# Kernel tuning notes

Hardware: AMD Instinct MI355X
Metric: run time of the kernel (lower is better)

## Reference

```python
import jax, jax.numpy as jnp
import numpy as np

ALPHA = 0.005
SCALE = 0.001
DELTA = 0.1
MAX_ITER = 50
EARLY = True


def setup_inputs() -> dict:
    key = jax.random.key(0)
    k1, k2, k3 = jax.random.split(key, 3)
    B, S, M, N = 32, 8, 512, 512
    x = jax.random.uniform(k1, (B, S, N), dtype=jnp.float32)
    A = jax.random.normal(k2, (B, S, M, N), dtype=jnp.float32) * 0.1
    b = jax.random.uniform(k3, (B, S, M), dtype=jnp.float32)
    return {"x": x, "A": A, "b": b}


def reference(x, A, b):
    # x: [B,S,N] primal iterate; A: [B,S,M,N] constraint matrices; b: [B,S,M]
    B, S = b.shape[0], b.shape[1]
    active0 = jnp.ones((B, S), dtype=bool)

    def body(carry, _):
        x_, active, stopped = carry
        # torch loop runs an iteration only while any(active) and not early-stopped
        run = jnp.any(active) & (~stopped)
        # Ax - b, clamped at 0 -> per-constraint violation
        Ax = jnp.einsum('bsn,bsmn->bsm', x_, A)          # [B,S,M]
        viol = jnp.clip(Ax - b, 0.0)
        new_active = jnp.sum(viol, axis=-1) >= DELTA      # ~(total < delta)
        stop_early = jnp.asarray(EARLY) & (~jnp.any(new_active))
        g = jnp.einsum('bsm,bsmn->bsn', viol, A)          # penalty gradient [B,S,N]
        lr = ALPHA / (1.0 + SCALE * g)
        x_upd = jnp.where(new_active[..., None], x_ - lr * g, x_)
        x_upd = jnp.clip(x_upd, 0.0)                      # clamp applied even to inactive rows
        # early stop happens BEFORE the update/clamp in the torch code
        x_new = jnp.where(stop_early, x_, x_upd)
        x_out = jnp.where(run, x_new, x_)
        active_out = jnp.where(run, new_active, active)
        stopped_out = stopped | (run & stop_early)
        return (x_out, active_out, stopped_out), None

    # torch: break when count > max_iter after increment -> up to max_iter+1 updates
    init = (x, active0, jnp.array(False))
    (x_final, _, _), _ = jax.lax.scan(body, init, None, length=MAX_ITER + 1)
    return x_final
```

## Files before the change

kernel.cpp:

```cpp
#include <hip/hip_runtime.h>

#define ALPHA 0.005f
#define SCALE 0.001f
#define DELTA 0.1f
#define MAXIT 51

constexpr int N = 512;
constexpr int M = 512;
constexpr int NTHREADS = 1024;
constexpr int NWAVES = NTHREADS / 64;
constexpr int MPW = M / NWAVES;
constexpr int NROWS = 256;
constexpr size_t WS_NEEDED = (size_t)NROWS * M * N * 2;

constexpr int CACHE_M0 = 416;
constexpr int CACHE_KK0 = 26;

template<int CTRL>
__device__ __forceinline__ float dpp_mov(float v) {
    return __int_as_float(__builtin_amdgcn_update_dpp(
        0, __float_as_int(v), CTRL, 0xF, 0xF, true));
}

__device__ __forceinline__ float wave_sum_u(float d) {
    d += dpp_mov<0x111>(d);
    d += dpp_mov<0x112>(d);
    d += dpp_mov<0x114>(d);
    d += dpp_mov<0x118>(d);
    d += dpp_mov<0x142>(d);
    d += dpp_mov<0x143>(d);
    return __int_as_float(__builtin_amdgcn_readlane(__float_as_int(d), 63));
}

__device__ __forceinline__ float dot8(const float4& a, const float4& c,
                                      const float4& xa, const float4& xb) {
    return a.x*xa.x + a.y*xa.y + a.z*xa.z + a.w*xa.w
         + c.x*xb.x + c.y*xb.y + c.z*xb.z + c.w*xb.w;
}

__device__ __forceinline__ unsigned pack2_bf16(float f0, float f1) {
    unsigned a = __float_as_uint(f0); a += 0x7fffu + ((a >> 16) & 1u);
    unsigned b = __float_as_uint(f1); b += 0x7fffu + ((b >> 16) & 1u);
    return (a >> 16) | (b & 0xffff0000u);
}
__device__ __forceinline__ float bflo(unsigned u) { return __uint_as_float(u << 16); }
__device__ __forceinline__ float bfhi(unsigned u) { return __uint_as_float(u & 0xffff0000u); }

__device__ __forceinline__ void unpack4(uint2 u, float4& f) {
    f.x = bflo(u.x); f.y = bfhi(u.x); f.z = bflo(u.y); f.w = bfhi(u.y);
}

__global__ __launch_bounds__(NTHREADS, 4)
void lva_bf16_kernel(const float* __restrict__ x_in,
                     const float* __restrict__ A,
                     const float* __restrict__ bvec,
                     float* __restrict__ x_out,
                     unsigned short* __restrict__ wsA)
{
    __shared__ __align__(16) float b_lds[M];
    __shared__ __align__(16) float g_lds[NWAVES * N];
    __shared__ float sv_lds[NWAVES];
    __shared__ int bc_active;
    __shared__ __align__(16) uint2 A_lds[96 * 128];

    const int tid  = threadIdx.x;
    const int lane = tid & 63;
    const int w    = tid >> 6;
    const int r    = blockIdx.x;

    if (tid < M) b_lds[tid] = bvec[(size_t)r * M + tid];

    const int n0 = lane * 4;
    const int n1 = 256 + lane * 4;

    const float* xrow = x_in + (size_t)r * N;
    float4 xa = *(const float4*)(xrow + n0);
    float4 xb = *(const float4*)(xrow + n1);

    const float* Ablk = A + (size_t)r * M * N + (size_t)w * N;
    unsigned short* Wblk = wsA + (size_t)r * M * N + (size_t)w * N;

    __syncthreads();

    bool alive = true;

    {
        float4 ga = make_float4(0.f, 0.f, 0.f, 0.f);
        float4 gb = make_float4(0.f, 0.f, 0.f, 0.f);
        float sviol = 0.f;

        #define STROW(j, aj, cj) do {                                               \
            if (kk + (j) >= CACHE_KK0) {                                            \
                const int rl = w + 16 * (kk + (j)) - CACHE_M0;                      \
                A_lds[rl * 128 + lane]      = make_uint2(pack2_bf16(aj.x, aj.y),    \
                                                         pack2_bf16(aj.z, aj.w));   \
                A_lds[rl * 128 + 64 + lane] = make_uint2(pack2_bf16(cj.x, cj.y),    \
                                                         pack2_bf16(cj.z, cj.w));   \
            } else {                                                                \
                unsigned short* q = Wblk + (size_t)(kk + (j)) * (16 * N);           \
                *(uint2*)(q + n0) = make_uint2(pack2_bf16(aj.x, aj.y),              \
                                               pack2_bf16(aj.z, aj.w));             \
                *(uint2*)(q + n1) = make_uint2(pack2_bf16(cj.x, cj.y),              \
                                               pack2_bf16(cj.z, cj.w));             \
            }                                                                       \
        } while (0)

        #pragma unroll 1
        for (int kk = 0; kk < MPW; kk += 4) {
            const float* p0 = Ablk + (size_t)(kk + 0) * (16 * N);
            const float* p1 = Ablk + (size_t)(kk + 1) * (16 * N);
            const float* p2 = Ablk + (size_t)(kk + 2) * (16 * N);
            const float* p3 = Ablk + (size_t)(kk + 3) * (16 * N);
            float4 a0 = *(const float4*)(p0 + n0), c0 = *(const float4*)(p0 + n1);
            float4 a1 = *(const float4*)(p1 + n0), c1 = *(const float4*)(p1 + n1);
            float4 a2 = *(const float4*)(p2 + n0), c2 = *(const float4*)(p2 + n1);
            float4 a3 = *(const float4*)(p3 + n0), c3 = *(const float4*)(p3 + n1);
            STROW(0, a0, c0); STROW(1, a1, c1); STROW(2, a2, c2); STROW(3, a3, c3);
            float bb0 = b_lds[w + 16 * (kk + 0)];
            float bb1 = b_lds[w + 16 * (kk + 1)];
            float bb2 = b_lds[w + 16 * (kk + 2)];
            float bb3 = b_lds[w + 16 * (kk + 3)];
            float d0 = wave_sum_u(dot8(a0, c0, xa, xb));
            float d1 = wave_sum_u(dot8(a1, c1, xa, xb));
            float d2 = wave_sum_u(dot8(a2, c2, xa, xb));
            float d3 = wave_sum_u(dot8(a3, c3, xa, xb));
            float v0 = fmaxf(d0 - bb0, 0.f);
            float v1 = fmaxf(d1 - bb1, 0.f);
            float v2 = fmaxf(d2 - bb2, 0.f);
            float v3 = fmaxf(d3 - bb3, 0.f);
            sviol += v0 + v1 + v2 + v3;
            ga.x += v0*a0.x + v1*a1.x + v2*a2.x + v3*a3.x;
            ga.y += v0*a0.y + v1*a1.y + v2*a2.y + v3*a3.y;
            ga.z += v0*a0.z + v1*a1.z + v2*a2.z + v3*a3.z;
            ga.w += v0*a0.w + v1*a1.w + v2*a2.w + v3*a3.w;
            gb.x += v0*c0.x + v1*c1.x + v2*c2.x + v3*c3.x;
            gb.y += v0*c0.y + v1*c1.y + v2*c2.y + v3*c3.y;
            gb.z += v0*c0.z + v1*c1.z + v2*c2.z + v3*c3.z;
            gb.w += v0*c0.w + v1*c1.w + v2*c2.w + v3*c3.w;
        }
        #undef STROW

        if (lane == 0) sv_lds[w] = sviol;
        *(float4*)(&g_lds[w * N + n0]) = ga;
        *(float4*)(&g_lds[w * N + n1]) = gb;
        __syncthreads();
        if (tid == 0) {
            float s = 0.f;
            #pragma unroll
            for (int i = 0; i < NWAVES; ++i) s += sv_lds[i];
            bc_active = (s >= DELTA) ? 1 : 0;
        }
        if (tid < N) {
            float s = 0.f;
            #pragma unroll
            for (int i = 0; i < NWAVES; ++i) s += g_lds[i * N + tid];
            g_lds[tid] = s;
        }
        __syncthreads();
        if (!bc_active) {
            alive = false;
        } else {
            float4 gfa = *(const float4*)(&g_lds[n0]);
            float4 gfb = *(const float4*)(&g_lds[n1]);
            xa.x = fmaxf(xa.x - (ALPHA / (1.f + SCALE*gfa.x)) * gfa.x, 0.f);
            xa.y = fmaxf(xa.y - (ALPHA / (1.f + SCALE*gfa.y)) * gfa.y, 0.f);
            xa.z = fmaxf(xa.z - (ALPHA / (1.f + SCALE*gfa.z)) * gfa.z, 0.f);
            xa.w = fmaxf(xa.w - (ALPHA / (1.f + SCALE*gfa.w)) * gfa.w, 0.f);
            xb.x = fmaxf(xb.x - (ALPHA / (1.f + SCALE*gfb.x)) * gfb.x, 0.f);
            xb.y = fmaxf(xb.y - (ALPHA / (1.f + SCALE*gfb.y)) * gfb.y, 0.f);
            xb.z = fmaxf(xb.z - (ALPHA / (1.f + SCALE*gfb.z)) * gfb.z, 0.f);
            xb.w = fmaxf(xb.w - (ALPHA / (1.f + SCALE*gfb.w)) * gfb.w, 0.f);
        }
    }

    const int h = lane >> 5;
    const int s = lane & 31;
    __syncthreads();
    if (w == 0) {
        *(float4*)(&g_lds[n0]) = xa;
        *(float4*)(&g_lds[n1]) = xb;
    }
    __syncthreads();
    float4 xf0 = *(const float4*)(&g_lds[  0 + s * 4]);
    float4 xf1 = *(const float4*)(&g_lds[128 + s * 4]);
    float4 xf2 = *(const float4*)(&g_lds[256 + s * 4]);
    float4 xf3 = *(const float4*)(&g_lds[384 + s * 4]);
    __syncthreads();

    if (alive) {
        const uint2* Wp = (const uint2*)(wsA + (size_t)r * M * N)
                          + (w + 16 * h) * 128 + s;
        const int mb = w + 16 * h;
        const int xadr = (lane ^ 32) << 2;

        uint2 c0, c1, c2, c3, p0, p1, p2, p3;

        #define LOADG(b0, b1, b2, b3, Gn) do {  \
            b0 = Wp[(Gn) * 4096];               \
            b1 = Wp[(Gn) * 4096 + 32];          \
            b2 = Wp[(Gn) * 4096 + 64];          \
            b3 = Wp[(Gn) * 4096 + 96];          \
        } while (0)

        #define COMPUTE(b0, b1, b2, b3, G) do {                               \
            float4 f0, f1, f2, f3;                                            \
            unpack4(b0, f0); unpack4(b1, f1);                                 \
            unpack4(b2, f2); unpack4(b3, f3);                                 \
            float d = f0.x*xf0.x + f0.y*xf0.y + f0.z*xf0.z + f0.w*xf0.w       \
                    + f1.x*xf1.x + f1.y*xf1.y + f1.z*xf1.z + f1.w*xf1.w       \
                    + f2.x*xf2.x + f2.y*xf2.y + f2.z*xf2.z + f2.w*xf2.w       \
                    + f3.x*xf3.x + f3.y*xf3.y + f3.z*xf3.z + f3.w*xf3.w;      \
            d += dpp_mov<0xB1>(d);            \
            d += dpp_mov<0x4E>(d);            \
            d += dpp_mov<0x141>(d);           \
            d += dpp_mov<0x140>(d);           \
            d += __int_as_float(__builtin_amdgcn_ds_swizzle(                  \
                     __float_as_int(d), 0x401F));        \
            float v = fmaxf(d - b_lds[mb + 32 * (G)], 0.f);                   \
            sviol += v;                                                       \
            g0.x += v*f0.x; g0.y += v*f0.y; g0.z += v*f0.z; g0.w += v*f0.w;   \
            g1.x += v*f1.x; g1.y += v*f1.y; g1.z += v*f1.z; g1.w += v*f1.w;   \
            g2.x += v*f2.x; g2.y += v*f2.y; g2.z += v*f2.z; g2.w += v*f2.w;   \
            g3.x += v*f3.x; g3.y += v*f3.y; g3.z += v*f3.z; g3.w += v*f3.w;   \
        } while (0)

        #define MRG(x) (x) += __int_as_float(                                 \
            __builtin_amdgcn_ds_bpermute(xadr, __float_as_int(x)))

        LOADG(c0, c1, c2, c3, 0);

        #pragma unroll 1
        for (int t = 1; t < MAXIT; ++t) {
            float4 g0 = make_float4(0.f, 0.f, 0.f, 0.f);
            float4 g1 = make_float4(0.f, 0.f, 0.f, 0.f);
            float4 g2 = make_float4(0.f, 0.f, 0.f, 0.f);
            float4 g3 = make_float4(0.f, 0.f, 0.f, 0.f);
            float sviol = 0.f;

            #pragma unroll 1
            for (int G = 0; G < 12; G += 2) {
                LOADG(p0, p1, p2, p3, G + 1);
                COMPUTE(c0, c1, c2, c3, G);
                LOADG(c0, c1, c2, c3, G + 2);
                COMPUTE(p0, p1, p2, p3, G + 1);
            }
            COMPUTE(c0, c1, c2, c3, 12);
            LOADG(c0, c1, c2, c3, 0);

            {
                const int base = mb * 128 + s;
                p0 = A_lds[base]; p1 = A_lds[base + 32];
                p2 = A_lds[base + 64]; p3 = A_lds[base + 96];
                COMPUTE(p0, p1, p2, p3, 13);
            }
            {
                const int base = (mb + 32) * 128 + s;
                p0 = A_lds[base]; p1 = A_lds[base + 32];
                p2 = A_lds[base + 64]; p3 = A_lds[base + 96];
                COMPUTE(p0, p1, p2, p3, 14);
            }
            {
                const int base = (mb + 64) * 128 + s;
                p0 = A_lds[base]; p1 = A_lds[base + 32];
                p2 = A_lds[base + 64]; p3 = A_lds[base + 96];
                COMPUTE(p0, p1, p2, p3, 15);
            }

            MRG(g0.x); MRG(g0.y); MRG(g0.z); MRG(g0.w);
            MRG(g1.x); MRG(g1.y); MRG(g1.z); MRG(g1.w);
            MRG(g2.x); MRG(g2.y); MRG(g2.z); MRG(g2.w);
            MRG(g3.x); MRG(g3.y); MRG(g3.z); MRG(g3.w);
            MRG(sviol);

            if (h == 0) {
                const int gb = w * N + s * 4;
                *(float4*)(&g_lds[gb      ]) = g0;
                *(float4*)(&g_lds[gb + 128]) = g1;
                *(float4*)(&g_lds[gb + 256]) = g2;
                *(float4*)(&g_lds[gb + 384]) = g3;
                if (s == 0) sv_lds[w] = sviol;
            }
            __syncthreads();
            if (tid == 0) {
                float sacc = 0.f;
                #pragma unroll
                for (int i = 0; i < NWAVES; ++i) sacc += sv_lds[i];
                bc_active = (sacc >= DELTA) ? 1 : 0;
            }
            if (tid < N) {
                float sacc = 0.f;
                #pragma unroll
                for (int i = 0; i < NWAVES; ++i) sacc += g_lds[i * N + tid];
                g_lds[tid] = sacc;
            }
            __syncthreads();
            if (!bc_active) break;

            float4 q0 = *(const float4*)(&g_lds[  0 + s * 4]);
            float4 q1 = *(const float4*)(&g_lds[128 + s * 4]);
            float4 q2 = *(const float4*)(&g_lds[256 + s * 4]);
            float4 q3 = *(const float4*)(&g_lds[384 + s * 4]);
            xf0.x = fmaxf(xf0.x - (ALPHA / (1.f + SCALE*q0.x)) * q0.x, 0.f);
            xf0.y = fmaxf(xf0.y - (ALPHA / (1.f + SCALE*q0.y)) * q0.y, 0.f);
            xf0.z = fmaxf(xf0.z - (ALPHA / (1.f + SCALE*q0.z)) * q0.z, 0.f);
            xf0.w = fmaxf(xf0.w - (ALPHA / (1.f + SCALE*q0.w)) * q0.w, 0.f);
            xf1.x = fmaxf(xf1.x - (ALPHA / (1.f + SCALE*q1.x)) * q1.x, 0.f);
            xf1.y = fmaxf(xf1.y - (ALPHA / (1.f + SCALE*q1.y)) * q1.y, 0.f);
            xf1.z = fmaxf(xf1.z - (ALPHA / (1.f + SCALE*q1.z)) * q1.z, 0.f);
            xf1.w = fmaxf(xf1.w - (ALPHA / (1.f + SCALE*q1.w)) * q1.w, 0.f);
            xf2.x = fmaxf(xf2.x - (ALPHA / (1.f + SCALE*q2.x)) * q2.x, 0.f);
            xf2.y = fmaxf(xf2.y - (ALPHA / (1.f + SCALE*q2.y)) * q2.y, 0.f);
            xf2.z = fmaxf(xf2.z - (ALPHA / (1.f + SCALE*q2.z)) * q2.z, 0.f);
            xf2.w = fmaxf(xf2.w - (ALPHA / (1.f + SCALE*q2.w)) * q2.w, 0.f);
            xf3.x = fmaxf(xf3.x - (ALPHA / (1.f + SCALE*q3.x)) * q3.x, 0.f);
            xf3.y = fmaxf(xf3.y - (ALPHA / (1.f + SCALE*q3.y)) * q3.y, 0.f);
            xf3.z = fmaxf(xf3.z - (ALPHA / (1.f + SCALE*q3.z)) * q3.z, 0.f);
            xf3.w = fmaxf(xf3.w - (ALPHA / (1.f + SCALE*q3.w)) * q3.w, 0.f);
            __syncthreads();
        }
        #undef LOADG
        #undef COMPUTE
        #undef MRG
    }

    if (w == 0 && h == 0) {
        float* orow = x_out + (size_t)r * N + s * 4;
        *(float4*)(orow +   0) = xf0;
        *(float4*)(orow + 128) = xf1;
        *(float4*)(orow + 256) = xf2;
        *(float4*)(orow + 384) = xf3;
    }
}

__global__ __launch_bounds__(NTHREADS, 4)
void lva_kernel(const float* __restrict__ x_in,
                const float* __restrict__ A,
                const float* __restrict__ bvec,
                float* __restrict__ x_out)
{
    __shared__ float b_lds[M];
    __shared__ float g_lds[NWAVES * N];
    __shared__ float sv_lds[NWAVES];
    __shared__ int bc_active;

    const int tid  = threadIdx.x;
    const int lane = tid & 63;
    const int w    = tid >> 6;
    const int r    = blockIdx.x;

    if (tid < M) b_lds[tid] = bvec[(size_t)r * M + tid];

    const int n0 = lane * 4;
    const int n1 = 256 + lane * 4;

    const float* xrow = x_in + (size_t)r * N;
    float4 xa = *(const float4*)(xrow + n0);
    float4 xb = *(const float4*)(xrow + n1);

    const float* Ablk = A + (size_t)r * M * N + (size_t)w * N;

    __syncthreads();

    for (int t = 0; t < MAXIT; ++t) {
        float4 ga = make_float4(0.f, 0.f, 0.f, 0.f);
        float4 gb = make_float4(0.f, 0.f, 0.f, 0.f);
        float sviol = 0.f;

        #pragma unroll 1
        for (int kk = 0; kk < MPW; kk += 4) {
            const float* p0 = Ablk + (size_t)(kk + 0) * (16 * N);
            const float* p1 = Ablk + (size_t)(kk + 1) * (16 * N);
            const float* p2 = Ablk + (size_t)(kk + 2) * (16 * N);
            const float* p3 = Ablk + (size_t)(kk + 3) * (16 * N);
            float4 a0 = *(const float4*)(p0 + n0), c0 = *(const float4*)(p0 + n1);
            float4 a1 = *(const float4*)(p1 + n0), c1 = *(const float4*)(p1 + n1);
            float4 a2 = *(const float4*)(p2 + n0), c2 = *(const float4*)(p2 + n1);
            float4 a3 = *(const float4*)(p3 + n0), c3 = *(const float4*)(p3 + n1);
            float bb0 = b_lds[w + 16 * (kk + 0)];
            float bb1 = b_lds[w + 16 * (kk + 1)];
            float bb2 = b_lds[w + 16 * (kk + 2)];
            float bb3 = b_lds[w + 16 * (kk + 3)];
            float d0 = wave_sum_u(dot8(a0, c0, xa, xb));
            float d1 = wave_sum_u(dot8(a1, c1, xa, xb));
            float d2 = wave_sum_u(dot8(a2, c2, xa, xb));
            float d3 = wave_sum_u(dot8(a3, c3, xa, xb));
            float v0 = fmaxf(d0 - bb0, 0.f);
            float v1 = fmaxf(d1 - bb1, 0.f);
            float v2 = fmaxf(d2 - bb2, 0.f);
            float v3 = fmaxf(d3 - bb3, 0.f);
            sviol += v0 + v1 + v2 + v3;
            ga.x += v0*a0.x + v1*a1.x + v2*a2.x + v3*a3.x;
            ga.y += v0*a0.y + v1*a1.y + v2*a2.y + v3*a3.y;
            ga.z += v0*a0.z + v1*a1.z + v2*a2.z + v3*a3.z;
            ga.w += v0*a0.w + v1*a1.w + v2*a2.w + v3*a3.w;
            gb.x += v0*c0.x + v1*c1.x + v2*c2.x + v3*c3.x;
            gb.y += v0*c0.y + v1*c1.y + v2*c2.y + v3*c3.y;
            gb.z += v0*c0.z + v1*c1.z + v2*c2.z + v3*c3.z;
            gb.w += v0*c0.w + v1*c1.w + v2*c2.w + v3*c3.w;
        }

        if (lane == 0) sv_lds[w] = sviol;
        *(float4*)(&g_lds[w * N + n0]) = ga;
        *(float4*)(&g_lds[w * N + n1]) = gb;
        __syncthreads();
        if (tid == 0) {
            float sacc = 0.f;
            #pragma unroll
            for (int i = 0; i < NWAVES; ++i) sacc += sv_lds[i];
            bc_active = (sacc >= DELTA) ? 1 : 0;
        }
        if (tid < N) {
            float sacc = 0.f;
            #pragma unroll
            for (int i = 0; i < NWAVES; ++i) sacc += g_lds[i * N + tid];
            g_lds[tid] = sacc;
        }
        __syncthreads();
        if (!bc_active) break;

        float4 gfa = *(const float4*)(&g_lds[n0]);
        float4 gfb = *(const float4*)(&g_lds[n1]);
        xa.x = fmaxf(xa.x - (ALPHA / (1.f + SCALE*gfa.x)) * gfa.x, 0.f);
        xa.y = fmaxf(xa.y - (ALPHA / (1.f + SCALE*gfa.y)) * gfa.y, 0.f);
        xa.z = fmaxf(xa.z - (ALPHA / (1.f + SCALE*gfa.z)) * gfa.z, 0.f);
        xa.w = fmaxf(xa.w - (ALPHA / (1.f + SCALE*gfa.w)) * gfa.w, 0.f);
        xb.x = fmaxf(xb.x - (ALPHA / (1.f + SCALE*gfb.x)) * gfb.x, 0.f);
        xb.y = fmaxf(xb.y - (ALPHA / (1.f + SCALE*gfb.y)) * gfb.y, 0.f);
        xb.z = fmaxf(xb.z - (ALPHA / (1.f + SCALE*gfb.z)) * gfb.z, 0.f);
        xb.w = fmaxf(xb.w - (ALPHA / (1.f + SCALE*gfb.w)) * gfb.w, 0.f);
        __syncthreads();
    }

    float* orow = x_out + (size_t)r * N;
    if (w == 0) {
        *(float4*)(orow + n0) = xa;
        *(float4*)(orow + n1) = xb;
    }
}

extern "C" void kernel_launch(void* const* d_in, const int* in_sizes, int n_in,
                              void* d_out, int out_size, void* d_ws, size_t ws_size,
                              hipStream_t stream)
{
    const float* x  = (const float*)d_in[0];
    const float* A  = (const float*)d_in[1];
    const float* b  = (const float*)d_in[2];
    float* out      = (float*)d_out;

    if (ws_size >= WS_NEEDED) {
        lva_bf16_kernel<<<dim3(NROWS), dim3(NTHREADS), 0, stream>>>(
            x, A, b, out, (unsigned short*)d_ws);
    } else {
        lva_kernel<<<dim3(NROWS), dim3(NTHREADS), 0, stream>>>(x, A, b, out);
    }
}
```

Before: 1.146 ms.

## Cache bf16 A rows in registers and LDS, cut workspace reads per iteration

```diff
diff --git a/kernel.cpp b/kernel.cpp
--- a/kernel.cpp
+++ b/kernel.cpp
@@ -13,8 +13,7 @@
 constexpr int NROWS = 256;
 constexpr size_t WS_NEEDED = (size_t)NROWS * M * N * 2;
 
-constexpr int CACHE_M0 = 416;
-constexpr int CACHE_KK0 = 26;
+constexpr int CACHE_M0 = 384;
 
 template<int CTRL>
 __device__ __forceinline__ float dpp_mov(float v) {
@@ -59,6 +58,7 @@
 {
     __shared__ __align__(16) float b_lds[M];
     __shared__ __align__(16) float g_lds[NWAVES * N];
+    __shared__ __align__(16) float gred[N];
     __shared__ float sv_lds[NWAVES];
     __shared__ int bc_active;
     __shared__ __align__(16) uint2 A_lds[96 * 128];
@@ -67,6 +67,9 @@
     const int lane = tid & 63;
     const int w    = tid >> 6;
     const int r    = blockIdx.x;
+    const int h    = lane >> 5;
+    const int s    = lane & 31;
+    const int xadr = (lane ^ 32) << 2;
 
     if (tid < M) b_lds[tid] = bvec[(size_t)r * M + tid];
 
@@ -83,85 +86,147 @@
     __syncthreads();
 
     bool alive = true;
+
+    uint2 q0a = make_uint2(0,0), q0b = q0a, q0c = q0a, q0d = q0a;
+    uint2 q1a = q0a, q1b = q0a, q1c = q0a, q1d = q0a;
+    uint2 q2a = q0a, q2b = q0a, q2c = q0a, q2d = q0a;
+    uint2 q3a = q0a, q3b = q0a, q3c = q0a, q3d = q0a;
+    uint2 q4a = q0a, q4b = q0a, q4c = q0a, q4d = q0a;
 
     {
         float4 ga = make_float4(0.f, 0.f, 0.f, 0.f);
         float4 gb = make_float4(0.f, 0.f, 0.f, 0.f);
         float sviol = 0.f;
-
-        #define STROW(j, aj, cj) do {                                               \
-            if (kk + (j) >= CACHE_KK0) {                                            \
-                const int rl = w + 16 * (kk + (j)) - CACHE_M0;                      \
-                A_lds[rl * 128 + lane]      = make_uint2(pack2_bf16(aj.x, aj.y),    \
-                                                         pack2_bf16(aj.z, aj.w));   \
-                A_lds[rl * 128 + 64 + lane] = make_uint2(pack2_bf16(cj.x, cj.y),    \
-                                                         pack2_bf16(cj.z, cj.w));   \
-            } else {                                                                \
-                unsigned short* q = Wblk + (size_t)(kk + (j)) * (16 * N);           \
-                *(uint2*)(q + n0) = make_uint2(pack2_bf16(aj.x, aj.y),              \
-                                               pack2_bf16(aj.z, aj.w));             \
-                *(uint2*)(q + n1) = make_uint2(pack2_bf16(cj.x, cj.y),              \
-                                               pack2_bf16(cj.z, cj.w));             \
-            }                                                                       \
+        float4 a0, a1, a2, a3, c0, c1, c2, c3;
+
+        #define LOADA4(KK) do {                                               \
+            const float* P0 = Ablk + (size_t)((KK) + 0) * (16 * N);           \
+            const float* P1 = Ablk + (size_t)((KK) + 1) * (16 * N);           \
+            const float* P2 = Ablk + (size_t)((KK) + 2) * (16 * N);           \
+            const float* P3 = Ablk + (size_t)((KK) + 3) * (16 * N);           \
+            a0 = *(const float4*)(P0 + n0); c0 = *(const float4*)(P0 + n1);   \
+            a1 = *(const float4*)(P1 + n0); c1 = *(const float4*)(P1 + n1);   \
+            a2 = *(const float4*)(P2 + n0); c2 = *(const float4*)(P2 + n1);   \
+            a3 = *(const float4*)(P3 + n0); c3 = *(const float4*)(P3 + n1);   \
+        } while (0)
+
+        #define DOTGRAD4(KK) do {                                             \
+            float bb0 = b_lds[w + 16 * ((KK) + 0)];                           \
+            float bb1 = b_lds[w + 16 * ((KK) + 1)];                           \
+            float bb2 = b_lds[w + 16 * ((KK) + 2)];                           \
+            float bb3 = b_lds[w + 16 * ((KK) + 3)];                           \
+            float d0 = wave_sum_u(dot8(a0, c0, xa, xb));                      \
+            float d1 = wave_sum_u(dot8(a1, c1, xa, xb));                      \
+            float d2 = wave_sum_u(dot8(a2, c2, xa, xb));                      \
+            float d3 = wave_sum_u(dot8(a3, c3, xa, xb));                      \
+            float v0 = fmaxf(d0 - bb0, 0.f);                                  \
+            float v1 = fmaxf(d1 - bb1, 0.f);                                  \
+            float v2 = fmaxf(d2 - bb2, 0.f);                                  \
+            float v3 = fmaxf(d3 - bb3, 0.f);                                  \
+            sviol += v0 + v1 + v2 + v3;                                       \
+            ga.x += v0*a0.x + v1*a1.x + v2*a2.x + v3*a3.x;                    \
+            ga.y += v0*a0.y + v1*a1.y + v2*a2.y + v3*a3.y;                    \
+            ga.z += v0*a0.z + v1*a1.z + v2*a2.z + v3*a3.z;                    \
+            ga.w += v0*a0.w + v1*a1.w + v2*a2.w + v3*a3.w;                    \
+            gb.x += v0*c0.x + v1*c1.x + v2*c2.x + v3*c3.x;                    \
+            gb.y += v0*c0.y + v1*c1.y + v2*c2.y + v3*c3.y;                    \
+            gb.z += v0*c0.z + v1*c1.z + v2*c2.z + v3*c3.z;                    \
+            gb.w += v0*c0.w + v1*c1.w + v2*c2.w + v3*c3.w;                    \
+        } while (0)
+
+        #define WS1(J, AJ, CJ) do {                                           \
+            unsigned short* q = Wblk + (size_t)(J) * (16 * N);                \
+            *(uint2*)(q + n0) = make_uint2(pack2_bf16(AJ.x, AJ.y),            \
+                                           pack2_bf16(AJ.z, AJ.w));           \
+            *(uint2*)(q + n1) = make_uint2(pack2_bf16(CJ.x, CJ.y),            \
+                                           pack2_bf16(CJ.z, CJ.w));           \
+        } while (0)
+
+        #define LDS1(J, AJ, CJ) do {                                          \
+            const int rl = w + 16 * (J) - CACHE_M0;                           \
+            A_lds[rl * 128 + lane]      = make_uint2(pack2_bf16(AJ.x, AJ.y),  \
+                                                     pack2_bf16(AJ.z, AJ.w)); \
+            A_lds[rl * 128 + 64 + lane] = make_uint2(pack2_bf16(CJ.x, CJ.y),  \
+                                                     pack2_bf16(CJ.z, CJ.w)); \
+        } while (0)
+
+        #define BPERM(v) (unsigned)__builtin_amdgcn_ds_bpermute(xadr, (int)(v))
+
+        #define CAPE(Q, AJ, CJ) do {                                          \
+            unsigned lo0 = pack2_bf16(AJ.x, AJ.y), lo1 = pack2_bf16(AJ.z, AJ.w); \
+            unsigned hi0 = pack2_bf16(CJ.x, CJ.y), hi1 = pack2_bf16(CJ.z, CJ.w); \
+            unsigned rl0 = BPERM(lo0), rl1 = BPERM(lo1);                      \
+            unsigned rh0 = BPERM(hi0), rh1 = BPERM(hi1);                      \
+            if (h == 0) {                                                     \
+                Q##a = make_uint2(lo0, lo1); Q##b = make_uint2(rl0, rl1);     \
+                Q##c = make_uint2(hi0, hi1); Q##d = make_uint2(rh0, rh1);     \
+            }                                                                 \
+        } while (0)
+        #define CAPO(Q, AJ, CJ) do {                                          \
+            unsigned lo0 = pack2_bf16(AJ.x, AJ.y), lo1 = pack2_bf16(AJ.z, AJ.w); \
+            unsigned hi0 = pack2_bf16(CJ.x, CJ.y), hi1 = pack2_bf16(CJ.z, CJ.w); \
+            unsigned rl0 = BPERM(lo0), rl1 = BPERM(lo1);                      \
+            unsigned rh0 = BPERM(hi0), rh1 = BPERM(hi1);                      \
+            if (h == 1) {                                                     \
+                Q##a = make_uint2(rl0, rl1); Q##b = make_uint2(lo0, lo1);     \
+                Q##c = make_uint2(rh0, rh1); Q##d = make_uint2(hi0, hi1);     \
+            }                                                                 \
         } while (0)
 
         #pragma unroll 1
-        for (int kk = 0; kk < MPW; kk += 4) {
-            const float* p0 = Ablk + (size_t)(kk + 0) * (16 * N);
-            const float* p1 = Ablk + (size_t)(kk + 1) * (16 * N);
-            const float* p2 = Ablk + (size_t)(kk + 2) * (16 * N);
-            const float* p3 = Ablk + (size_t)(kk + 3) * (16 * N);
-            float4 a0 = *(const float4*)(p0 + n0), c0 = *(const float4*)(p0 + n1);
-            float4 a1 = *(const float4*)(p1 + n0), c1 = *(const float4*)(p1 + n1);
-            float4 a2 = *(const float4*)(p2 + n0), c2 = *(const float4*)(p2 + n1);
-            float4 a3 = *(const float4*)(p3 + n0), c3 = *(const float4*)(p3 + n1);
-            STROW(0, a0, c0); STROW(1, a1, c1); STROW(2, a2, c2); STROW(3, a3, c3);
-            float bb0 = b_lds[w + 16 * (kk + 0)];
-            float bb1 = b_lds[w + 16 * (kk + 1)];
-            float bb2 = b_lds[w + 16 * (kk + 2)];
-            float bb3 = b_lds[w + 16 * (kk + 3)];
-            float d0 = wave_sum_u(dot8(a0, c0, xa, xb));
-            float d1 = wave_sum_u(dot8(a1, c1, xa, xb));
-            float d2 = wave_sum_u(dot8(a2, c2, xa, xb));
-            float d3 = wave_sum_u(dot8(a3, c3, xa, xb));
-            float v0 = fmaxf(d0 - bb0, 0.f);
-            float v1 = fmaxf(d1 - bb1, 0.f);
-            float v2 = fmaxf(d2 - bb2, 0.f);
-            float v3 = fmaxf(d3 - bb3, 0.f);
-            sviol += v0 + v1 + v2 + v3;
-            ga.x += v0*a0.x + v1*a1.x + v2*a2.x + v3*a3.x;
-            ga.y += v0*a0.y + v1*a1.y + v2*a2.y + v3*a3.y;
-            ga.z += v0*a0.z + v1*a1.z + v2*a2.z + v3*a3.z;
-            ga.w += v0*a0.w + v1*a1.w + v2*a2.w + v3*a3.w;
-            gb.x += v0*c0.x + v1*c1.x + v2*c2.x + v3*c3.x;
-            gb.y += v0*c0.y + v1*c1.y + v2*c2.y + v3*c3.y;
-            gb.z += v0*c0.z + v1*c1.z + v2*c2.z + v3*c3.z;
-            gb.w += v0*c0.w + v1*c1.w + v2*c2.w + v3*c3.w;
-        }
-        #undef STROW
+        for (int kk = 0; kk < 16; kk += 4) {
+            LOADA4(kk);
+            WS1(kk + 0, a0, c0); WS1(kk + 1, a1, c1);
+            WS1(kk + 2, a2, c2); WS1(kk + 3, a3, c3);
+            DOTGRAD4(kk);
+        }
+        LOADA4(16);
+        CAPE(q0, a0, c0); CAPO(q0, a1, c1);
+        CAPE(q1, a2, c2); CAPO(q1, a3, c3);
+        DOTGRAD4(16);
+        LOADA4(20);
+        CAPE(q2, a0, c0); CAPO(q2, a1, c1);
+        CAPE(q3, a2, c2); CAPO(q3, a3, c3);
+        DOTGRAD4(20);
+        LOADA4(24);
+        LDS1(24, a0, c0); LDS1(25, a1, c1);
+        LDS1(26, a2, c2); LDS1(27, a3, c3);
+        DOTGRAD4(24);
+        LOADA4(28);
+        LDS1(28, a0, c0); LDS1(29, a1, c1);
+        CAPE(q4, a2, c2); CAPO(q4, a3, c3);
+        DOTGRAD4(28);
+
+        #undef LOADA4
+        #undef WS1
+        #undef LDS1
+        #undef CAPE
+        #undef CAPO
+        #undef BPERM
+        #undef DOTGRAD4
 
         if (lane == 0) sv_lds[w] = sviol;
         *(float4*)(&g_lds[w * N + n0]) = ga;
         *(float4*)(&g_lds[w * N + n1]) = gb;
         __syncthreads();
         if (tid == 0) {
-            float s = 0.f;
+            float sacc = 0.f;
             #pragma unroll
-            for (int i = 0; i < NWAVES; ++i) s += sv_lds[i];
-            bc_active = (s >= DELTA) ? 1 : 0;
+            for (int i = 0; i < NWAVES; ++i) sacc += sv_lds[i];
+            bc_active = (sacc >= DELTA) ? 1 : 0;
         }
         if (tid < N) {
-            float s = 0.f;
+            float sacc = 0.f;
             #pragma unroll
-            for (int i = 0; i < NWAVES; ++i) s += g_lds[i * N + tid];
-            g_lds[tid] = s;
+            for (int i = 0; i < NWAVES; ++i) sacc += g_lds[i * N + tid];
+            gred[tid] = sacc;
         }
         __syncthreads();
         if (!bc_active) {
             alive = false;
         } else {
-            float4 gfa = *(const float4*)(&g_lds[n0]);
-            float4 gfb = *(const float4*)(&g_lds[n1]);
+            float4 gfa = *(const float4*)(&gred[n0]);
+            float4 gfb = *(const float4*)(&gred[n1]);
             xa.x = fmaxf(xa.x - (ALPHA / (1.f + SCALE*gfa.x)) * gfa.x, 0.f);
             xa.y = fmaxf(xa.y - (ALPHA / (1.f + SCALE*gfa.y)) * gfa.y, 0.f);
             xa.z = fmaxf(xa.z - (ALPHA / (1.f + SCALE*gfa.z)) * gfa.z, 0.f);
@@ -173,8 +238,6 @@
         }
     }
 
-    const int h = lane >> 5;
-    const int s = lane & 31;
     __syncthreads();
     if (w == 0) {
         *(float4*)(&g_lds[n0]) = xa;
@@ -191,7 +254,6 @@
         const uint2* Wp = (const uint2*)(wsA + (size_t)r * M * N)
                           + (w + 16 * h) * 128 + s;
         const int mb = w + 16 * h;
-        const int xadr = (lane ^ 32) << 2;
 
         uint2 c0, c1, c2, c3, p0, p1, p2, p3;
 
@@ -237,34 +299,40 @@
             float4 g3 = make_float4(0.f, 0.f, 0.f, 0.f);
             float sviol = 0.f;
 
-            #pragma unroll 1
-            for (int G = 0; G < 12; G += 2) {
-                LOADG(p0, p1, p2, p3, G + 1);
-                COMPUTE(c0, c1, c2, c3, G);
-                LOADG(c0, c1, c2, c3, G + 2);
-                COMPUTE(p0, p1, p2, p3, G + 1);
-            }
-            COMPUTE(c0, c1, c2, c3, 12);
-            LOADG(c0, c1, c2, c3, 0);
+            LOADG(p0, p1, p2, p3, 1); COMPUTE(c0, c1, c2, c3, 0);
+            LOADG(c0, c1, c2, c3, 2); COMPUTE(p0, p1, p2, p3, 1);
+            LOADG(p0, p1, p2, p3, 3); COMPUTE(c0, c1, c2, c3, 2);
+            LOADG(c0, c1, c2, c3, 4); COMPUTE(p0, p1, p2, p3, 3);
+            LOADG(p0, p1, p2, p3, 5); COMPUTE(c0, c1, c2, c3, 4);
+            LOADG(c0, c1, c2, c3, 6); COMPUTE(p0, p1, p2, p3, 5);
+            LOADG(p0, p1, p2, p3, 7); COMPUTE(c0, c1, c2, c3, 6);
+            LOADG(c0, c1, c2, c3, 0); COMPUTE(p0, p1, p2, p3, 7);
+
+            COMPUTE(q0a, q0b, q0c, q0d,  8);
+            COMPUTE(q1a, q1b, q1c, q1d,  9);
+            COMPUTE(q2a, q2b, q2c, q2d, 10);
+            COMPUTE(q3a, q3b, q3c, q3d, 11);
 
             {
                 const int base = mb * 128 + s;
+                p0 = A_lds[base]; p1 = A_lds[base + 32];
+                p2 = A_lds[base + 64]; p3 = A_lds[base + 96];
+                COMPUTE(p0, p1, p2, p3, 12);
+            }
+            {
+                const int base = (mb + 32) * 128 + s;
                 p0 = A_lds[base]; p1 = A_lds[base + 32];
                 p2 = A_lds[base + 64]; p3 = A_lds[base + 96];
                 COMPUTE(p0, p1, p2, p3, 13);
             }
             {
-                const int base = (mb + 32) * 128 + s;
+                const int base = (mb + 64) * 128 + s;
                 p0 = A_lds[base]; p1 = A_lds[base + 32];
                 p2 = A_lds[base + 64]; p3 = A_lds[base + 96];
                 COMPUTE(p0, p1, p2, p3, 14);
             }
-            {
-                const int base = (mb + 64) * 128 + s;
-                p0 = A_lds[base]; p1 = A_lds[base + 32];
-                p2 = A_lds[base + 64]; p3 = A_lds[base + 96];
-                COMPUTE(p0, p1, p2, p3, 15);
-            }
+
+            COMPUTE(q4a, q4b, q4c, q4d, 15);
 
             MRG(g0.x); MRG(g0.y); MRG(g0.z); MRG(g0.w);
             MRG(g1.x); MRG(g1.y); MRG(g1.z); MRG(g1.w);
@@ -291,15 +359,15 @@
                 float sacc = 0.f;
                 #pragma unroll
                 for (int i = 0; i < NWAVES; ++i) sacc += g_lds[i * N + tid];
-                g_lds[tid] = sacc;
+                gred[tid] = sacc;
             }
             __syncthreads();
             if (!bc_active) break;
 
-            float4 q0 = *(const float4*)(&g_lds[  0 + s * 4]);
-            float4 q1 = *(const float4*)(&g_lds[128 + s * 4]);
-            float4 q2 = *(const float4*)(&g_lds[256 + s * 4]);
-            float4 q3 = *(const float4*)(&g_lds[384 + s * 4]);
+            float4 q0 = *(const float4*)(&gred[  0 + s * 4]);
+            float4 q1 = *(const float4*)(&gred[128 + s * 4]);
+            float4 q2 = *(const float4*)(&gred[256 + s * 4]);
+            float4 q3 = *(const float4*)(&gred[384 + s * 4]);
             xf0.x = fmaxf(xf0.x - (ALPHA / (1.f + SCALE*q0.x)) * q0.x, 0.f);
             xf0.y = fmaxf(xf0.y - (ALPHA / (1.f + SCALE*q0.y)) * q0.y, 0.f);
             xf0.z = fmaxf(xf0.z - (ALPHA / (1.f + SCALE*q0.z)) * q0.z, 0.f);
@@ -316,7 +384,6 @@
             xf3.y = fmaxf(xf3.y - (ALPHA / (1.f + SCALE*q3.y)) * q3.y, 0.f);
             xf3.z = fmaxf(xf3.z - (ALPHA / (1.f + SCALE*q3.z)) * q3.z, 0.f);
             xf3.w = fmaxf(xf3.w - (ALPHA / (1.f + SCALE*q3.w)) * q3.w, 0.f);
-            __syncthreads();
         }
         #undef LOADG
         #undef COMPUTE
```

Result: slower. 3.682 ms (+221.2%).

## Split each problem row across two cooperative blocks with global gradient exchange

Applied to the files above, without the earlier changes.

```diff
diff --git a/kernel.cpp b/kernel.cpp
--- a/kernel.cpp
+++ b/kernel.cpp
@@ -1,4 +1,5 @@
 #include <hip/hip_runtime.h>
+#include <hip/hip_cooperative_groups.h>
 
 #define ALPHA 0.005f
 #define SCALE 0.001f
@@ -12,9 +13,6 @@
 constexpr int MPW = M / NWAVES;
 constexpr int NROWS = 256;
 constexpr size_t WS_NEEDED = (size_t)NROWS * M * N * 2;
-
-constexpr int CACHE_M0 = 416;
-constexpr int CACHE_KK0 = 26;
 
 template<int CTRL>
 __device__ __forceinline__ float dpp_mov(float v) {
@@ -49,6 +47,328 @@
 __device__ __forceinline__ void unpack4(uint2 u, float4& f) {
     f.x = bflo(u.x); f.y = bfhi(u.x); f.z = bflo(u.y); f.w = bfhi(u.y);
 }
+
+__global__ __launch_bounds__(NTHREADS, 8)
+void lva_bf16_split(const float* __restrict__ x_in,
+                    const float* __restrict__ A,
+                    const float* __restrict__ bvec,
+                    float* __restrict__ x_out,
+                    unsigned short* __restrict__ wsA)
+{
+    __shared__ __align__(16) float b_lds[256];
+    __shared__ __align__(16) float g_lds[NWAVES * N];
+    __shared__ __align__(16) float gred[N];
+    __shared__ __align__(16) float xswap[N];
+    __shared__ float sv_lds[NWAVES];
+    __shared__ float sv_tot[2];
+    __shared__ __align__(16) uint2 A_lds[32 * 128];
+
+    const int tid  = threadIdx.x;
+    const int lane = tid & 63;
+    const int w    = tid >> 6;
+    const int bid  = blockIdx.x;
+    const int r    = bid >> 1;
+    const int q    = bid & 1;
+    const int h    = lane >> 5;
+    const int s    = lane & 31;
+    const int xadr = (lane ^ 32) << 2;
+
+    float* H  = (float*)(wsA + (size_t)r * M * N + 224 * N);
+    int* TK   = (int*)(H + 4 * 513);
+    float* XP[2] = { H + (0 * 2 + q) * 513, H + (1 * 2 + q) * 513 };
+    float* PP[2] = { H + (0 * 2 + (q ^ 1)) * 513, H + (1 * 2 + (q ^ 1)) * 513 };
+
+    if (tid < 52)
+        __hip_atomic_store(&TK[tid], 0, __ATOMIC_RELAXED, __HIP_MEMORY_SCOPE_AGENT);
+    cooperative_groups::this_grid().sync();
+
+    if (tid < 256) b_lds[tid] = bvec[(size_t)r * M + q * 256 + tid];
+
+    const int n0 = lane * 4;
+    const int n1 = 256 + lane * 4;
+
+    const float* xrow = x_in + (size_t)r * N;
+    float4 xa = *(const float4*)(xrow + n0);
+    float4 xb = *(const float4*)(xrow + n1);
+
+    const float* Ablk = A + (size_t)r * M * N + (size_t)(q * 256 + w) * N;
+    unsigned short* Wblk = wsA + (size_t)r * M * N + (size_t)(q * 256 + w) * N;
+
+    __syncthreads();
+
+    bool alive = true;
+    float svt;
+
+    #define EXCHG(T) do {                                                     \
+        __syncthreads();                                            \
+        if (tid < N) {                                                        \
+            float sacc = 0.f;                                                 \
+            _Pragma("unroll")                                                 \
+            for (int i = 0; i < NWAVES; ++i) sacc += g_lds[i * N + tid];      \
+            gred[tid] = sacc;                                                 \
+            __hip_atomic_store(&XP[(T) & 1][tid], sacc,                       \
+                               __ATOMIC_RELAXED, __HIP_MEMORY_SCOPE_AGENT);   \
+        }                                                                     \
+        if (tid == 0) {                                                       \
+            float sv = 0.f;                                                   \
+            _Pragma("unroll")                                                 \
+            for (int i = 0; i < NWAVES; ++i) sv += sv_lds[i];                 \
+            sv_tot[0] = sv;                                                   \
+            __hip_atomic_store(&XP[(T) & 1][N], sv,                           \
+                               __ATOMIC_RELAXED, __HIP_MEMORY_SCOPE_AGENT);   \
+        }                                                                     \
+        __syncthreads();                                            \
+        if (tid == 0) {                                                       \
+            __threadfence();                                                  \
+            int my = __hip_atomic_fetch_add(&TK[(T)], 1,                      \
+                         __ATOMIC_ACQ_REL, __HIP_MEMORY_SCOPE_AGENT);         \
+            int tgt = (my | 1) + 1;                                           \
+            while (__hip_atomic_load(&TK[(T)], __ATOMIC_ACQUIRE,              \
+                                     __HIP_MEMORY_SCOPE_AGENT) < tgt)         \
+                __builtin_amdgcn_s_sleep(1);                                  \
+            __threadfence();                                                  \
+        }                                                                     \
+        __syncthreads();                                            \
+        if (tid < N) {                                                        \
+            float pv = __hip_atomic_load(&PP[(T) & 1][tid],                   \
+                           __ATOMIC_RELAXED, __HIP_MEMORY_SCOPE_AGENT);       \
+            gred[tid] += pv;                                                  \
+        }                                                                     \
+        if (tid == N) {                                                       \
+            sv_tot[1] = __hip_atomic_load(&PP[(T) & 1][N],                    \
+                            __ATOMIC_RELAXED, __HIP_MEMORY_SCOPE_AGENT);      \
+        }                                                                     \
+        __syncthreads();                                            \
+        svt = sv_tot[0] + sv_tot[1];                                          \
+    } while (0)
+
+    {
+        float4 ga = make_float4(0.f, 0.f, 0.f, 0.f);
+        float4 gb = make_float4(0.f, 0.f, 0.f, 0.f);
+        float sviol = 0.f;
+        float4 a0, a1, a2, a3, c0, c1, c2, c3;
+
+        #define LOADA4(KK) do {                                               \
+            const float* P0 = Ablk + (size_t)((KK) + 0) * (16 * N);           \
+            const float* P1 = Ablk + (size_t)((KK) + 1) * (16 * N);           \
+            const float* P2 = Ablk + (size_t)((KK) + 2) * (16 * N);           \
+            const float* P3 = Ablk + (size_t)((KK) + 3) * (16 * N);           \
+            a0 = *(const float4*)(P0 + n0); c0 = *(const float4*)(P0 + n1);   \
+            a1 = *(const float4*)(P1 + n0); c1 = *(const float4*)(P1 + n1);   \
+            a2 = *(const float4*)(P2 + n0); c2 = *(const float4*)(P2 + n1);   \
+            a3 = *(const float4*)(P3 + n0); c3 = *(const float4*)(P3 + n1);   \
+        } while (0)
+
+        #define DOTGRAD4(KK) do {                                             \
+            float bb0 = b_lds[w + 16 * ((KK) + 0)];                           \
+            float bb1 = b_lds[w + 16 * ((KK) + 1)];                           \
+            float bb2 = b_lds[w + 16 * ((KK) + 2)];                           \
+            float bb3 = b_lds[w + 16 * ((KK) + 3)];                           \
+            float d0 = wave_sum_u(dot8(a0, c0, xa, xb));                      \
+            float d1 = wave_sum_u(dot8(a1, c1, xa, xb));                      \
+            float d2 = wave_sum_u(dot8(a2, c2, xa, xb));                      \
+            float d3 = wave_sum_u(dot8(a3, c3, xa, xb));                      \
+            float v0 = fmaxf(d0 - bb0, 0.f);                                  \
+            float v1 = fmaxf(d1 - bb1, 0.f);                                  \
+            float v2 = fmaxf(d2 - bb2, 0.f);                                  \
+            float v3 = fmaxf(d3 - bb3, 0.f);                                  \
+            sviol += v0 + v1 + v2 + v3;                                       \
+            ga.x += v0*a0.x + v1*a1.x + v2*a2.x + v3*a3.x;                    \
+            ga.y += v0*a0.y + v1*a1.y + v2*a2.y + v3*a3.y;                    \
+            ga.z += v0*a0.z + v1*a1.z + v2*a2.z + v3*a3.z;                    \
+            ga.w += v0*a0.w + v1*a1.w + v2*a2.w + v3*a3.w;                    \
+            gb.x += v0*c0.x + v1*c1.x + v2*c2.x + v3*c3.x;                    \
+            gb.y += v0*c0.y + v1*c1.y + v2*c2.y + v3*c3.y;                    \
+            gb.z += v0*c0.z + v1*c1.z + v2*c2.z + v3*c3.z;                    \
+            gb.w += v0*c0.w + v1*c1.w + v2*c2.w + v3*c3.w;                    \
+        } while (0)
+
+        #define WS1(J, AJ, CJ) do {                                           \
+            unsigned short* qq = Wblk + (size_t)(J) * (16 * N);               \
+            *(uint2*)(qq + n0) = make_uint2(pack2_bf16(AJ.x, AJ.y),           \
+                                            pack2_bf16(AJ.z, AJ.w));          \
+            *(uint2*)(qq + n1) = make_uint2(pack2_bf16(CJ.x, CJ.y),           \
+                                            pack2_bf16(CJ.z, CJ.w));          \
+        } while (0)
+
+        #define LDS1(J, AJ, CJ) do {                                          \
+            const int rl = w + 16 * (J) - 224;                                \
+            A_lds[rl * 128 + lane]      = make_uint2(pack2_bf16(AJ.x, AJ.y),  \
+                                                     pack2_bf16(AJ.z, AJ.w)); \
+            A_lds[rl * 128 + 64 + lane] = make_uint2(pack2_bf16(CJ.x, CJ.y),  \
+                                                     pack2_bf16(CJ.z, CJ.w)); \
+        } while (0)
+
+        #pragma unroll 1
+        for (int kk = 0; kk < 12; kk += 4) {
+            LOADA4(kk);
+            WS1(kk + 0, a0, c0); WS1(kk + 1, a1, c1);
+            WS1(kk + 2, a2, c2); WS1(kk + 3, a3, c3);
+            DOTGRAD4(kk);
+        }
+        LOADA4(12);
+        WS1(12, a0, c0); WS1(13, a1, c1);
+        LDS1(14, a2, c2); LDS1(15, a3, c3);
+        DOTGRAD4(12);
+
+        #undef LOADA4
+        #undef WS1
+        #undef LDS1
+        #undef DOTGRAD4
+
+        if (lane == 0) sv_lds[w] = sviol;
+        *(float4*)(&g_lds[w * N + n0]) = ga;
+        *(float4*)(&g_lds[w * N + n1]) = gb;
+
+        EXCHG(0);
+
+        if (svt < DELTA) {
+            alive = false;
+        } else {
+            float4 gfa = *(const float4*)(&gred[n0]);
+            float4 gfb = *(const float4*)(&gred[n1]);
+            xa.x = fmaxf(xa.x - (ALPHA / (1.f + SCALE*gfa.x)) * gfa.x, 0.f);
+            xa.y = fmaxf(xa.y - (ALPHA / (1.f + SCALE*gfa.y)) * gfa.y, 0.f);
+            xa.z = fmaxf(xa.z - (ALPHA / (1.f + SCALE*gfa.z)) * gfa.z, 0.f);
+            xa.w = fmaxf(xa.w - (ALPHA / (1.f + SCALE*gfa.w)) * gfa.w, 0.f);
+            xb.x = fmaxf(xb.x - (ALPHA / (1.f + SCALE*gfb.x)) * gfb.x, 0.f);
+            xb.y = fmaxf(xb.y - (ALPHA / (1.f + SCALE*gfb.y)) * gfb.y, 0.f);
+            xb.z = fmaxf(xb.z - (ALPHA / (1.f + SCALE*gfb.z)) * gfb.z, 0.f);
+            xb.w = fmaxf(xb.w - (ALPHA / (1.f + SCALE*gfb.w)) * gfb.w, 0.f);
+        }
+    }
+
+    if (w == 0) {
+        *(float4*)(&xswap[n0]) = xa;
+        *(float4*)(&xswap[n1]) = xb;
+    }
+    __syncthreads();
+    float4 xf0 = *(const float4*)(&xswap[  0 + s * 4]);
+    float4 xf1 = *(const float4*)(&xswap[128 + s * 4]);
+    float4 xf2 = *(const float4*)(&xswap[256 + s * 4]);
+    float4 xf3 = *(const float4*)(&xswap[384 + s * 4]);
+
+    if (alive) {
+        const int mb = w + 16 * h;
+        const uint2* Wp = (const uint2*)(wsA + (size_t)r * M * N)
+                          + (q * 256 + mb) * 128 + s;
+
+        uint2 c0, c1, c2, c3, p0, p1, p2, p3;
+
+        #define LOADG(b0, b1, b2, b3, Gn) do {  \
+            b0 = Wp[(Gn) * 4096];               \
+            b1 = Wp[(Gn) * 4096 + 32];          \
+            b2 = Wp[(Gn) * 4096 + 64];          \
+            b3 = Wp[(Gn) * 4096 + 96];          \
+        } while (0)
+
+        #define COMPUTE(b0, b1, b2, b3, G) do {                               \
+            float4 f0, f1, f2, f3;                                            \
+            unpack4(b0, f0); unpack4(b1, f1);                                 \
+            unpack4(b2, f2); unpack4(b3, f3);                                 \
+            float d = f0.x*xf0.x + f0.y*xf0.y + f0.z*xf0.z + f0.w*xf0.w       \
+                    + f1.x*xf1.x + f1.y*xf1.y + f1.z*xf1.z + f1.w*xf1.w       \
+                    + f2.x*xf2.x + f2.y*xf2.y + f2.z*xf2.z + f2.w*xf2.w       \
+                    + f3.x*xf3.x + f3.y*xf3.y + f3.z*xf3.z + f3.w*xf3.w;      \
+            d += dpp_mov<0xB1>(d);                                  \
+            d += dpp_mov<0x4E>(d);                                  \
+            d += dpp_mov<0x141>(d);                                 \
+            d += dpp_mov<0x140>(d);                                 \
+            d += __int_as_float(__builtin_amdgcn_ds_swizzle(                  \
+                     __float_as_int(d), 0x401F));        \
+            float v = fmaxf(d - b_lds[mb + 32 * (G)], 0.f);                   \
+            sviol += v;                                                       \
+            g0.x += v*f0.x; g0.y += v*f0.y; g0.z += v*f0.z; g0.w += v*f0.w;   \
+            g1.x += v*f1.x; g1.y += v*f1.y; g1.z += v*f1.z; g1.w += v*f1.w;   \
+            g2.x += v*f2.x; g2.y += v*f2.y; g2.z += v*f2.z; g2.w += v*f2.w;   \
+            g3.x += v*f3.x; g3.y += v*f3.y; g3.z += v*f3.z; g3.w += v*f3.w;   \
+        } while (0)
+
+        #define MRG(x) (x) += __int_as_float(                                 \
+            __builtin_amdgcn_ds_bpermute(xadr, __float_as_int(x)))
+
+        LOADG(c0, c1, c2, c3, 0);
+
+        #pragma unroll 1
+        for (int t = 1; t < MAXIT; ++t) {
+            float4 g0 = make_float4(0.f, 0.f, 0.f, 0.f);
+            float4 g1 = make_float4(0.f, 0.f, 0.f, 0.f);
+            float4 g2 = make_float4(0.f, 0.f, 0.f, 0.f);
+            float4 g3 = make_float4(0.f, 0.f, 0.f, 0.f);
+            float sviol = 0.f;
+
+            LOADG(p0, p1, p2, p3, 1); COMPUTE(c0, c1, c2, c3, 0);
+            LOADG(c0, c1, c2, c3, 2); COMPUTE(p0, p1, p2, p3, 1);
+            LOADG(p0, p1, p2, p3, 3); COMPUTE(c0, c1, c2, c3, 2);
+            LOADG(c0, c1, c2, c3, 4); COMPUTE(p0, p1, p2, p3, 3);
+            LOADG(p0, p1, p2, p3, 5); COMPUTE(c0, c1, c2, c3, 4);
+            LOADG(c0, c1, c2, c3, 6); COMPUTE(p0, p1, p2, p3, 5);
+            COMPUTE(c0, c1, c2, c3, 6);
+            LOADG(c0, c1, c2, c3, 0);
+
+            {
+                const int base = mb * 128 + s;
+                p0 = A_lds[base]; p1 = A_lds[base + 32];
+                p2 = A_lds[base + 64]; p3 = A_lds[base + 96];
+                COMPUTE(p0, p1, p2, p3, 7);
+            }
+
+            MRG(g0.x); MRG(g0.y); MRG(g0.z); MRG(g0.w);
+            MRG(g1.x); MRG(g1.y); MRG(g1.z); MRG(g1.w);
+            MRG(g2.x); MRG(g2.y); MRG(g2.z); MRG(g2.w);
+            MRG(g3.x); MRG(g3.y); MRG(g3.z); MRG(g3.w);
+            MRG(sviol);
+
+            if (h == 0) {
+                const int gb_ = w * N + s * 4;
+                *(float4*)(&g_lds[gb_      ]) = g0;
+                *(float4*)(&g_lds[gb_ + 128]) = g1;
+                *(float4*)(&g_lds[gb_ + 256]) = g2;
+                *(float4*)(&g_lds[gb_ + 384]) = g3;
+                if (s == 0) sv_lds[w] = sviol;
+            }
+
+            EXCHG(t);
+
+            if (svt < DELTA) break;
+
+            float4 q0 = *(const float4*)(&gred[  0 + s * 4]);
+            float4 q1 = *(const float4*)(&gred[128 + s * 4]);
+            float4 q2 = *(const float4*)(&gred[256 + s * 4]);
+            float4 q3 = *(const float4*)(&gred[384 + s * 4]);
+            xf0.x = fmaxf(xf0.x - (ALPHA / (1.f + SCALE*q0.x)) * q0.x, 0.f);
+            xf0.y = fmaxf(xf0.y - (ALPHA / (1.f + SCALE*q0.y)) * q0.y, 0.f);
+            xf0.z = fmaxf(xf0.z - (ALPHA / (1.f + SCALE*q0.z)) * q0.z, 0.f);
+            xf0.w = fmaxf(xf0.w - (ALPHA / (1.f + SCALE*q0.w)) * q0.w, 0.f);
+            xf1.x = fmaxf(xf1.x - (ALPHA / (1.f + SCALE*q1.x)) * q1.x, 0.f);
+            xf1.y = fmaxf(xf1.y - (ALPHA / (1.f + SCALE*q1.y)) * q1.y, 0.f);
+            xf1.z = fmaxf(xf1.z - (ALPHA / (1.f + SCALE*q1.z)) * q1.z, 0.f);
+            xf1.w = fmaxf(xf1.w - (ALPHA / (1.f + SCALE*q1.w)) * q1.w, 0.f);
+            xf2.x = fmaxf(xf2.x - (ALPHA / (1.f + SCALE*q2.x)) * q2.x, 0.f);
+            xf2.y = fmaxf(xf2.y - (ALPHA / (1.f + SCALE*q2.y)) * q2.y, 0.f);
+            xf2.z = fmaxf(xf2.z - (ALPHA / (1.f + SCALE*q2.z)) * q2.z, 0.f);
+            xf2.w = fmaxf(xf2.w - (ALPHA / (1.f + SCALE*q2.w)) * q2.w, 0.f);
+            xf3.x = fmaxf(xf3.x - (ALPHA / (1.f + SCALE*q3.x)) * q3.x, 0.f);
+            xf3.y = fmaxf(xf3.y - (ALPHA / (1.f + SCALE*q3.y)) * q3.y, 0.f);
+            xf3.z = fmaxf(xf3.z - (ALPHA / (1.f + SCALE*q3.z)) * q3.z, 0.f);
+            xf3.w = fmaxf(xf3.w - (ALPHA / (1.f + SCALE*q3.w)) * q3.w, 0.f);
+        }
+        #undef LOADG
+        #undef COMPUTE
+        #undef MRG
+    }
+    #undef EXCHG
+
+    if (q == 0 && w == 0 && h == 0) {
+        float* orow = x_out + (size_t)r * N + s * 4;
+        *(float4*)(orow +   0) = xf0;
+        *(float4*)(orow + 128) = xf1;
+        *(float4*)(orow + 256) = xf2;
+        *(float4*)(orow + 384) = xf3;
+    }
+}
+
+constexpr int CACHE_M0 = 416;
 
 __global__ __launch_bounds__(NTHREADS, 4)
 void lva_bf16_kernel(const float* __restrict__ x_in,
@@ -90,18 +410,18 @@
         float sviol = 0.f;
 
         #define STROW(j, aj, cj) do {                                               \
-            if (kk + (j) >= CACHE_KK0) {                                            \
+            if (kk + (j) >= 26) {                                                   \
                 const int rl = w + 16 * (kk + (j)) - CACHE_M0;                      \
                 A_lds[rl * 128 + lane]      = make_uint2(pack2_bf16(aj.x, aj.y),    \
                                                          pack2_bf16(aj.z, aj.w));   \
                 A_lds[rl * 128 + 64 + lane] = make_uint2(pack2_bf16(cj.x, cj.y),    \
                                                          pack2_bf16(cj.z, cj.w));   \
             } else {                                                                \
-                unsigned short* q = Wblk + (size_t)(kk + (j)) * (16 * N);           \
-                *(uint2*)(q + n0) = make_uint2(pack2_bf16(aj.x, aj.y),              \
-                                               pack2_bf16(aj.z, aj.w));             \
-                *(uint2*)(q + n1) = make_uint2(pack2_bf16(cj.x, cj.y),              \
-                                               pack2_bf16(cj.z, cj.w));             \
+                unsigned short* qq = Wblk + (size_t)(kk + (j)) * (16 * N);          \
+                *(uint2*)(qq + n0) = make_uint2(pack2_bf16(aj.x, aj.y),             \
+                                                pack2_bf16(aj.z, aj.w));            \
+                *(uint2*)(qq + n1) = make_uint2(pack2_bf16(cj.x, cj.y),             \
+                                                pack2_bf16(cj.z, cj.w));            \
             }                                                                       \
         } while (0)
 
@@ -145,16 +465,16 @@
         *(float4*)(&g_lds[w * N + n1]) = gb;
         __syncthreads();
         if (tid == 0) {
-            float s = 0.f;
+            float s_ = 0.f;
             #pragma unroll
-            for (int i = 0; i < NWAVES; ++i) s += sv_lds[i];
-            bc_active = (s >= DELTA) ? 1 : 0;
+            for (int i = 0; i < NWAVES; ++i) s_ += sv_lds[i];
+            bc_active = (s_ >= DELTA) ? 1 : 0;
         }
         if (tid < N) {
-            float s = 0.f;
+            float s_ = 0.f;
             #pragma unroll
-            for (int i = 0; i < NWAVES; ++i) s += g_lds[i * N + tid];
-            g_lds[tid] = s;
+            for (int i = 0; i < NWAVES; ++i) s_ += g_lds[i * N + tid];
+            g_lds[tid] = s_;
         }
         __syncthreads();
         if (!bc_active) {
@@ -175,6 +495,7 @@
 
     const int h = lane >> 5;
     const int s = lane & 31;
+    const int xadr = (lane ^ 32) << 2;
     __syncthreads();
     if (w == 0) {
         *(float4*)(&g_lds[n0]) = xa;
@@ -191,7 +512,6 @@
         const uint2* Wp = (const uint2*)(wsA + (size_t)r * M * N)
                           + (w + 16 * h) * 128 + s;
         const int mb = w + 16 * h;
-        const int xadr = (lane ^ 32) << 2;
 
         uint2 c0, c1, c2, c3, p0, p1, p2, p3;
 
@@ -210,12 +530,12 @@
                     + f1.x*xf1.x + f1.y*xf1.y + f1.z*xf1.z + f1.w*xf1.w       \
                     + f2.x*xf2.x + f2.y*xf2.y + f2.z*xf2.z + f2.w*xf2.w       \
                     + f3.x*xf3.x + f3.y*xf3.y + f3.z*xf3.z + f3.w*xf3.w;      \
-            d += dpp_mov<0xB1>(d);            \
-            d += dpp_mov<0x4E>(d);            \
-            d += dpp_mov<0x141>(d);           \
-            d += dpp_mov<0x140>(d);           \
+            d += dpp_mov<0xB1>(d);                                            \
+            d += dpp_mov<0x4E>(d);                                            \
+            d += dpp_mov<0x141>(d);                                           \
+            d += dpp_mov<0x140>(d);                                           \
             d += __int_as_float(__builtin_amdgcn_ds_swizzle(                  \
-                     __float_as_int(d), 0x401F));        \
+                     __float_as_int(d), 0x401F));                             \
             float v = fmaxf(d - b_lds[mb + 32 * (G)], 0.f);                   \
             sviol += v;                                                       \
             g0.x += v*f0.x; g0.y += v*f0.y; g0.z += v*f0.z; g0.w += v*f0.w;   \
@@ -273,11 +593,11 @@
             MRG(sviol);
 
             if (h == 0) {
-                const int gb = w * N + s * 4;
-                *(float4*)(&g_lds[gb      ]) = g0;
-                *(float4*)(&g_lds[gb + 128]) = g1;
-                *(float4*)(&g_lds[gb + 256]) = g2;
-                *(float4*)(&g_lds[gb + 384]) = g3;
+                const int gb_ = w * N + s * 4;
+                *(float4*)(&g_lds[gb_      ]) = g0;
+                *(float4*)(&g_lds[gb_ + 128]) = g1;
+                *(float4*)(&g_lds[gb_ + 256]) = g2;
+                *(float4*)(&g_lds[gb_ + 384]) = g3;
                 if (s == 0) sv_lds[w] = sviol;
             }
             __syncthreads();
@@ -287,19 +607,20 @@
                 for (int i = 0; i < NWAVES; ++i) sacc += sv_lds[i];
                 bc_active = (sacc >= DELTA) ? 1 : 0;
             }
+            __syncthreads();
             if (tid < N) {
                 float sacc = 0.f;
                 #pragma unroll
                 for (int i = 0; i < NWAVES; ++i) sacc += g_lds[i * N + tid];
-                g_lds[tid] = sacc;
+                g_lds[NWAVES * N - N + tid] = sacc;
             }
             __syncthreads();
             if (!bc_active) break;
 
-            float4 q0 = *(const float4*)(&g_lds[  0 + s * 4]);
-            float4 q1 = *(const float4*)(&g_lds[128 + s * 4]);
-            float4 q2 = *(const float4*)(&g_lds[256 + s * 4]);
-            float4 q3 = *(const float4*)(&g_lds[384 + s * 4]);
+            float4 q0 = *(const float4*)(&g_lds[NWAVES * N - N +   0 + s * 4]);
+            float4 q1 = *(const float4*)(&g_lds[NWAVES * N - N + 128 + s * 4]);
+            float4 q2 = *(const float4*)(&g_lds[NWAVES * N - N + 256 + s * 4]);
+            float4 q3 = *(const float4*)(&g_lds[NWAVES * N - N + 384 + s * 4]);
             xf0.x = fmaxf(xf0.x - (ALPHA / (1.f + SCALE*q0.x)) * q0.x, 0.f);
             xf0.y = fmaxf(xf0.y - (ALPHA / (1.f + SCALE*q0.y)) * q0.y, 0.f);
             xf0.z = fmaxf(xf0.z - (ALPHA / (1.f + SCALE*q0.z)) * q0.z, 0.f);
@@ -448,8 +769,23 @@
     float* out      = (float*)d_out;
 
     if (ws_size >= WS_NEEDED) {
+        unsigned short* ws = (unsigned short*)d_ws;
+        int maxb = 0;
+        hipError_t oe = hipOccupancyMaxActiveBlocksPerMultiprocessor(
+            &maxb, lva_bf16_split, NTHREADS, 0);
+        if (oe == hipSuccess && maxb >= 2) {
+            void* kargs[] = { (void*)&x, (void*)&A, (void*)&b,
+                              (void*)&out, (void*)&ws };
+            hipError_t e = hipLaunchCooperativeKernel(
+                (void*)lva_bf16_split, dim3(2 * NROWS), dim3(NTHREADS),
+                kargs, 0, stream);
+            if (e == hipSuccess) return;
+            (void)hipGetLastError();
+        } else {
+            (void)hipGetLastError();
+        }
         lva_bf16_kernel<<<dim3(NROWS), dim3(NTHREADS), 0, stream>>>(
-            x, A, b, out, (unsigned short*)d_ws);
+            x, A, b, out, ws);
     } else {
         lva_kernel<<<dim3(NROWS), dim3(NTHREADS), 0, stream>>>(x, A, b, out);
     }
```

After: 1.118 ms. -2.4%, faster.
